# Performance work log

Measured on AMD Instinct MI355X. Metric: run time of the kernel, lower is better.

## Reference

```python
import jax, jax.numpy as jnp
import numpy as np

B, H, S, D = 4, 16, 2048, 64
SCALE = 8.0  # sqrt(D)
NEG = -1000000000.0


def setup_inputs() -> dict:
    key = jax.random.key(0)
    kq, kk, kv = jax.random.split(key, 3)
    q = jax.random.normal(kq, (B, H, S, D), dtype=jnp.float32)
    k = jax.random.normal(kk, (B, H, S, D), dtype=jnp.float32)
    v = jax.random.normal(kv, (B, H, S, D), dtype=jnp.float32)
    # causal mask: True means masked out (matches torch masked_fill)
    mask = jnp.triu(jnp.ones((S, S), dtype=bool), k=1)[None, None, :, :]
    mask = jnp.broadcast_to(mask, (B, 1, S, S))
    return {"q": q, "k": k, "v": v, "mask": mask}


def reference(q, k, v, mask):
    # score = q @ k^T / scale  -> [B,H,S,S]
    score = jnp.einsum("bhqd,bhkd->bhqk", q, k) / SCALE
    score = jnp.where(mask, NEG, score)
    probs = jax.nn.softmax(score, axis=-1)
    context = jnp.einsum("bhqk,bhkd->bhqd", probs, v)
    return context
```

## Files before the change

kernel.cpp:

```cpp
#include <hip/hip_runtime.h>

#define SQ 2048
#define DH 64
#define BK 64
#define NQT 32
#define NBH 64
#define M0 8.0f

#define WS_BYTES ((size_t)2 * NBH * SQ * DH * 2)

typedef float f32x4 __attribute__((ext_vector_type(4)));
typedef __bf16 bf16x8 __attribute__((ext_vector_type(8)));
typedef _Float16 f16x4 __attribute__((ext_vector_type(4)));
typedef __fp16 fp16x2 __attribute__((ext_vector_type(2)));
typedef unsigned short u16x8 __attribute__((ext_vector_type(8)));
typedef unsigned int u32x4 __attribute__((ext_vector_type(4)));

static __device__ __forceinline__ unsigned int pkbf(float a, float b) {
#if __has_builtin(__builtin_amdgcn_cvt_pk_bf16_f32)
  typedef __bf16 bf16x2 __attribute__((ext_vector_type(2)));
  bf16x2 r = __builtin_amdgcn_cvt_pk_bf16_f32(a, b);
  return __builtin_bit_cast(unsigned int, r);
#else
  unsigned int ua = __builtin_bit_cast(unsigned int, a);
  unsigned int ub = __builtin_bit_cast(unsigned int, b);
  ua += 0x7fffu + ((ua >> 16) & 1u);
  ub += 0x7fffu + ((ub >> 16) & 1u);
  return (ua >> 16) | (ub & 0xffff0000u);
#endif
}

static __device__ __forceinline__ unsigned int pkf16(float a, float b) {
  fp16x2 r = __builtin_amdgcn_cvt_pkrtz(a, b);
  return __builtin_bit_cast(unsigned int, r);
}

static __device__ __forceinline__ f32x4 mfma_qk(u16x8 a, u16x8 b, f32x4 c) {
  return __builtin_amdgcn_mfma_f32_16x16x32_bf16(
      __builtin_bit_cast(bf16x8, a), __builtin_bit_cast(bf16x8, b), c, 0, 0, 0);
}

static __device__ __forceinline__ f32x4 mfma_pv(f16x4 a, f16x4 b, f32x4 c) {
  return __builtin_amdgcn_mfma_f32_16x16x16f16(a, b, c, 0, 0, 0);
}

static __device__ __forceinline__ void ld16(unsigned short* l, const unsigned short* g) {
  __builtin_amdgcn_global_load_lds(
      (const __attribute__((address_space(1))) unsigned int*)(const void*)g,
      (__attribute__((address_space(3))) unsigned int*)(void*)l, 16, 0, 0);
}

static __device__ __forceinline__ void store_tile(float* wb, float* dst,
                                                  const f32x4* o, int lane,
                                                  int l15, int quad) {
#pragma unroll
  for (int dt = 0; dt < 4; ++dt) {
    const int colw = dt * 16 + quad * 4;
    *(f32x4*)&wb[l15 * 64 + (colw ^ ((l15 & 3) * 16))] = o[dt];
  }
  __builtin_amdgcn_wave_barrier();
#pragma unroll
  for (int j = 0; j < 4; ++j) {
    const int row = j * 4 + (lane >> 4);
    const int colw = (lane & 15) * 4;
    f32x4 v = *(const f32x4*)&wb[row * 64 + (colw ^ ((row & 3) * 16))];
    *(f32x4*)&dst[row * 64 + colw] = v;
  }
}

__global__ __launch_bounds__(256) void prep(const float* __restrict__ K,
                                            const float* __restrict__ V,
                                            unsigned short* __restrict__ Kb,
                                            unsigned short* __restrict__ Vt) {
  const int bh = (int)blockIdx.x >> 5;
  const int st = (int)blockIdx.x & 31;
  const int tid = threadIdx.x;
  __shared__ __align__(16) unsigned short T[DH * 64];
  {
    const int r = tid >> 2, c0 = (tid & 3) * 16;
    const float* kp = K + ((size_t)bh * SQ + st * 64 + r) * DH + c0;
    f32x4 x0 = *(const f32x4*)kp, x1 = *(const f32x4*)(kp + 4),
          x2 = *(const f32x4*)(kp + 8), x3 = *(const f32x4*)(kp + 12);
    u32x4 w0 = {pkbf(x0[0], x0[1]), pkbf(x0[2], x0[3]), pkbf(x1[0], x1[1]), pkbf(x1[2], x1[3])};
    u32x4 w1 = {pkbf(x2[0], x2[1]), pkbf(x2[2], x2[3]), pkbf(x3[0], x3[1]), pkbf(x3[2], x3[3])};
    unsigned short* kb = Kb + ((size_t)bh * SQ + st * 64 + r) * DH + c0;
    *(u32x4*)kb = w0;
    *(u32x4*)(kb + 8) = w1;
  }
  {
    const int kvb = (tid >> 4) * 4, vdb = (tid & 15) * 4;
    const float* vp = V + ((size_t)bh * SQ + st * 64 + kvb) * DH + vdb;
    f32x4 r0 = *(const f32x4*)vp, r1 = *(const f32x4*)(vp + DH),
          r2 = *(const f32x4*)(vp + 2 * DH), r3 = *(const f32x4*)(vp + 3 * DH);
    const int uu = kvb >> 3, h = (kvb >> 2) & 1;
#pragma unroll
    for (int i = 0; i < 4; ++i) {
      const int d = vdb + i;
      uint2 w = {pkf16(r0[i], r1[i]), pkf16(r2[i], r3[i])};
      *(uint2*)&T[d * 64 + ((uu ^ (d & 7)) * 8) + h * 4] = w;
    }
  }
  __syncthreads();
  {
    const int d2 = tid >> 2, cp = (tid & 3) * 2;
#pragma unroll
    for (int e = 0; e < 2; ++e) {
      const int uu = cp + e;
      u16x8 val = *(const u16x8*)&T[d2 * 64 + ((uu ^ (d2 & 7)) * 8)];
      *(u16x8*)&Vt[(size_t)bh * DH * SQ + (size_t)d2 * SQ + st * 64 + uu * 8] = val;
    }
  }
}

__global__ __launch_bounds__(256, 4) void fa_main(
    const float* __restrict__ Q, const unsigned short* __restrict__ Kb,
    const unsigned short* __restrict__ Vt, float* __restrict__ O) {
  const int lin = (int)blockIdx.x;
  const int xcd = lin & 7, u = lin >> 3;
  const int hh = u & 7;
  const int pi = (int)((0x32104567BA98CDEFull >> ((u >> 3) * 4)) & 15u);
  const int bh = hh * 8 + xcd;
  const int tend = 2 * pi + 1;

  const int tid = threadIdx.x;
  const int wv = tid >> 6;
  const int lane = tid & 63;
  const int l15 = lane & 15;
  const int quad = lane >> 4;

  __shared__ __align__(16) unsigned short S0[2 * BK * DH];
  __shared__ __align__(16) unsigned short S1[2 * BK * DH];

  const size_t hq = (size_t)bh * (SQ * DH);
  const unsigned short* KbH = Kb + (size_t)bh * SQ * DH;
  const unsigned short* VtH = Vt + (size_t)bh * DH * SQ;

  const int srow = wv * 16 + (lane >> 3);
  const int sc = lane & 7;

  const int qbase = pi * 128 + wv * 32;
  const int dtw = 2 * pi + (wv >> 1);
  const int qo = (wv & 1) * 32;

  u16x8 qf[2][2];
  {
    const float scq = 0.125f * 1.4426950408889634f;
#pragma unroll
    for (int f = 0; f < 2; ++f) {
      const float* qp = Q + hq + (size_t)(qbase + 16 * f + l15) * DH + quad * 8;
#pragma unroll
      for (int c = 0; c < 2; ++c) {
        f32x4 x = *(const f32x4*)(qp + c * 32);
        f32x4 y = *(const f32x4*)(qp + c * 32 + 4);
        u32x4 w = {pkbf(x[0] * scq, x[1] * scq), pkbf(x[2] * scq, x[3] * scq),
                   pkbf(y[0] * scq, y[1] * scq), pkbf(y[2] * scq, y[3] * scq)};
        qf[f][c] = __builtin_bit_cast(u16x8, w);
      }
    }
  }

  f32x4 o0[4], o1[4], la0, la1;
#pragma unroll
  for (int dt = 0; dt < 4; ++dt) {
    o0[dt] = (f32x4){0.f, 0.f, 0.f, 0.f};
    o1[dt] = (f32x4){0.f, 0.f, 0.f, 0.f};
  }
  la0 = (f32x4){0.f, 0.f, 0.f, 0.f};
  la1 = (f32x4){0.f, 0.f, 0.f, 0.f};
  const f16x4 ones = {(_Float16)1.f, (_Float16)1.f, (_Float16)1.f, (_Float16)1.f};

  auto stage = [&](unsigned short* W, int t) {
    const int kb = t * BK;
    unsigned short* Kd = W;
    unsigned short* Vd = W + BK * DH;
#pragma unroll
    for (int j = 0; j < 2; ++j) {
      const int row = srow + j * 8;
      ld16(&Kd[row * 64 + sc * 8], &KbH[(size_t)(kb + row) * 64 + ((sc ^ (row & 7)) * 8)]);
      ld16(&Vd[row * 64 + sc * 8], &VtH[(size_t)row * SQ + kb + ((sc ^ (row & 7)) * 8)]);
    }
  };

  auto attend = [&](const unsigned short* R, bool diag) {
    const unsigned short* Ks = R;
    const unsigned short* Vs = R + BK * DH;
    f32x4 s0[4], s1[4];
#pragma unroll
    for (int nt = 0; nt < 4; ++nt) {
      f32x4 a0 = {-M0, -M0, -M0, -M0}, a1 = {-M0, -M0, -M0, -M0};
#pragma unroll
      for (int c = 0; c < 2; ++c) {
        const int row = nt * 16 + l15;
        const int un = c * 4 + quad;
        u16x8 kf = *(const u16x8*)&Ks[row * 64 + ((un ^ (row & 7)) * 8)];
        a0 = mfma_qk(kf, qf[0][c], a0);
        a1 = mfma_qk(kf, qf[1][c], a1);
      }
      s0[nt] = a0;
      s1[nt] = a1;
    }
    if (diag) {
#pragma unroll
      for (int nt = 0; nt < 4; ++nt)
#pragma unroll
        for (int r = 0; r < 4; ++r) {
          const int kvl = nt * 16 + quad * 4 + r;
          if (kvl > qo + l15) s0[nt][r] = -1e30f;
          if (kvl > qo + 16 + l15) s1[nt][r] = -1e30f;
        }
    }
    f16x4 pf0[4], pf1[4];
#pragma unroll
    for (int nt = 0; nt < 4; ++nt) {
      f32x4 p0, p1;
#pragma unroll
      for (int r = 0; r < 4; ++r) {
        p0[r] = __builtin_amdgcn_exp2f(s0[nt][r]);
        p1[r] = __builtin_amdgcn_exp2f(s1[nt][r]);
      }
      uint2 w0 = {pkf16(p0[0], p0[1]), pkf16(p0[2], p0[3])};
      uint2 w1 = {pkf16(p1[0], p1[1]), pkf16(p1[2], p1[3])};
      pf0[nt] = __builtin_bit_cast(f16x4, w0);
      pf1[nt] = __builtin_bit_cast(f16x4, w1);
    }
#pragma unroll
    for (int nt = 0; nt < 4; ++nt) {
      la0 = mfma_pv(ones, pf0[nt], la0);
      la1 = mfma_pv(ones, pf1[nt], la1);
    }
#pragma unroll
    for (int dt = 0; dt < 4; ++dt) {
      const int d = dt * 16 + l15;
#pragma unroll
      for (int nt = 0; nt < 4; ++nt) {
        const int uv = nt * 2 + (quad >> 1);
        f16x4 vf = *(const f16x4*)&Vs[d * 64 + ((uv ^ (d & 7)) * 8) + (quad & 1) * 4];
        o0[dt] = mfma_pv(vf, pf0[nt], o0[dt]);
        o1[dt] = mfma_pv(vf, pf1[nt], o1[dt]);
      }
    }
  };

  auto step = [&](int t, const unsigned short* R, unsigned short* W) {
    if (t <= dtw) attend(R, t == dtw);
    __syncthreads();
    if (t + 2 <= tend) stage(W, t + 2);
  };

  stage(S0, 0);
  __syncthreads();
  stage(S1, 1);
  for (int t = 0; t <= tend; t += 2) {
    step(t, S0, S0);
    if (t + 1 <= tend) step(t + 1, S1, S1);
  }

  float* wb = (float*)S0 + wv * 1024;
  {
    const float inv = 1.0f / la0[0];
    f32x4 on[4];
#pragma unroll
    for (int dt = 0; dt < 4; ++dt) on[dt] = o0[dt] * inv;
    store_tile(wb, O + hq + (size_t)(qbase)*DH, on, lane, l15, quad);
  }
  {
    const float inv = 1.0f / la1[0];
    f32x4 on[4];
#pragma unroll
    for (int dt = 0; dt < 4; ++dt) on[dt] = o1[dt] * inv;
    store_tile(wb, O + hq + (size_t)(qbase + 16) * DH, on, lane, l15, quad);
  }
}

__global__ __launch_bounds__(256, 4) void fa_full(
    const float* __restrict__ Q, const float* __restrict__ K,
    const float* __restrict__ V, float* __restrict__ O) {
  const int lin = (int)blockIdx.x;
  const int xcd = lin & 7;
  const int u = lin >> 3;
  const int hh = u & 7;
  const int p = u >> 3;
  const int bh = hh * 8 + xcd;
  const int tid = threadIdx.x;
  const int wv = tid >> 6;
  const int lane = tid & 63;
  const int l15 = lane & 15;
  const int quad = lane >> 4;
  __shared__ __align__(16) unsigned short SMEM[2][2 * BK * DH];
  const size_t hbase = (size_t)bh * (SQ * DH);
  const int krr = tid >> 3, kcc = (tid & 7) * 8;
  const int kvb = (tid >> 4) * 4, vdb = (tid & 15) * 4;
#pragma unroll
  for (int ph = 0; ph < 2; ++ph) {
    const int qt = ph ? (NQT - 1 - p) : p;
    const int wq0 = qt * 64 + wv * 16;
    u16x8 qf[2];
    {
      const float scq = 0.125f * 1.4426950408889634f;
      const float* qp = Q + hbase + (size_t)(wq0 + l15) * DH + quad * 8;
#pragma unroll
      for (int c = 0; c < 2; ++c) {
        f32x4 x = *(const f32x4*)(qp + c * 32);
        f32x4 y = *(const f32x4*)(qp + c * 32 + 4);
        u32x4 w = {pkbf(x[0] * scq, x[1] * scq), pkbf(x[2] * scq, x[3] * scq),
                   pkbf(y[0] * scq, y[1] * scq), pkbf(y[2] * scq, y[3] * scq)};
        qf[c] = __builtin_bit_cast(u16x8, w);
      }
    }
    f32x4 o[4];
#pragma unroll
    for (int dt = 0; dt < 4; ++dt) o[dt] = (f32x4){0.f, 0.f, 0.f, 0.f};
    float l = 0.f;
    f32x4 ka[2][2], va[4];
    {
      const float* kp = K + hbase + (size_t)krr * DH + kcc;
      ka[0][0] = *(const f32x4*)kp;             ka[0][1] = *(const f32x4*)(kp + 4);
      ka[1][0] = *(const f32x4*)(kp + 32 * DH); ka[1][1] = *(const f32x4*)(kp + 32 * DH + 4);
      const float* vp = V + hbase + (size_t)kvb * DH + vdb;
      va[0] = *(const f32x4*)vp;            va[1] = *(const f32x4*)(vp + DH);
      va[2] = *(const f32x4*)(vp + 2 * DH); va[3] = *(const f32x4*)(vp + 3 * DH);
    }
    __syncthreads();
    {
      unsigned short* Ksn = SMEM[0];
      unsigned short* Vsn = SMEM[0] + BK * DH;
#pragma unroll
      for (int h = 0; h < 2; ++h) {
        const int rr = h * 32 + krr;
        u32x4 w = {pkbf(ka[h][0][0], ka[h][0][1]), pkbf(ka[h][0][2], ka[h][0][3]),
                   pkbf(ka[h][1][0], ka[h][1][1]), pkbf(ka[h][1][2], ka[h][1][3])};
        *(u32x4*)&Ksn[rr * DH + (kcc ^ ((rr & 7) * 8))] = w;
      }
#pragma unroll
      for (int i = 0; i < 4; ++i) {
        const int d = vdb + i;
        uint2 w = {pkf16(va[0][i], va[1][i]), pkf16(va[2][i], va[3][i])};
        *(uint2*)&Vsn[d * BK + (kvb ^ ((d & 15) * 4))] = w;
      }
    }
    __syncthreads();
    for (int t = 0; t <= qt; ++t) {
      const unsigned short* Ks = SMEM[t & 1];
      const unsigned short* Vs = SMEM[t & 1] + BK * DH;
      if (t < qt) {
        const int kb2 = (t + 1) * BK;
        const float* kp = K + hbase + (size_t)(kb2 + krr) * DH + kcc;
        ka[0][0] = *(const f32x4*)kp;             ka[0][1] = *(const f32x4*)(kp + 4);
        ka[1][0] = *(const f32x4*)(kp + 32 * DH); ka[1][1] = *(const f32x4*)(kp + 32 * DH + 4);
        const float* vp = V + hbase + (size_t)(kb2 + kvb) * DH + vdb;
        va[0] = *(const f32x4*)vp;            va[1] = *(const f32x4*)(vp + DH);
        va[2] = *(const f32x4*)(vp + 2 * DH); va[3] = *(const f32x4*)(vp + 3 * DH);
      }
      f32x4 s[4];
#pragma unroll
      for (int nt = 0; nt < 4; ++nt) {
        f32x4 acc = {-M0, -M0, -M0, -M0};
#pragma unroll
        for (int c = 0; c < 2; ++c) {
          const int row = nt * 16 + l15;
          u16x8 kf = *(const u16x8*)&Ks[row * DH + ((c * 32 + quad * 8) ^ ((l15 & 7) * 8))];
          acc = mfma_qk(kf, qf[c], acc);
        }
        s[nt] = acc;
      }
      if (t == qt) {
#pragma unroll
        for (int nt = 0; nt < 4; ++nt)
#pragma unroll
          for (int r = 0; r < 4; ++r)
            if (nt * 16 + quad * 4 + r > wv * 16 + l15) s[nt][r] = -1e30f;
      }
      f16x4 pf[4];
#pragma unroll
      for (int nt = 0; nt < 4; ++nt) {
        f32x4 pr;
#pragma unroll
        for (int r = 0; r < 4; ++r) { pr[r] = __builtin_amdgcn_exp2f(s[nt][r]); l += pr[r]; }
        uint2 w2 = {pkf16(pr[0], pr[1]), pkf16(pr[2], pr[3])};
        pf[nt] = __builtin_bit_cast(f16x4, w2);
      }
#pragma unroll
      for (int dt = 0; dt < 4; ++dt) {
        const int d = dt * 16 + l15;
#pragma unroll
        for (int nt = 0; nt < 4; ++nt) {
          f16x4 vf = *(const f16x4*)&Vs[d * BK + ((nt * 16 + quad * 4) ^ (l15 * 4))];
          o[dt] = mfma_pv(vf, pf[nt], o[dt]);
        }
      }
      if (t < qt) {
        unsigned short* Ksn = SMEM[(t + 1) & 1];
        unsigned short* Vsn = SMEM[(t + 1) & 1] + BK * DH;
#pragma unroll
        for (int h = 0; h < 2; ++h) {
          const int rr = h * 32 + krr;
          u32x4 w = {pkbf(ka[h][0][0], ka[h][0][1]), pkbf(ka[h][0][2], ka[h][0][3]),
                     pkbf(ka[h][1][0], ka[h][1][1]), pkbf(ka[h][1][2], ka[h][1][3])};
          *(u32x4*)&Ksn[rr * DH + (kcc ^ ((rr & 7) * 8))] = w;
        }
#pragma unroll
        for (int i = 0; i < 4; ++i) {
          const int d = vdb + i;
          uint2 w = {pkf16(va[0][i], va[1][i]), pkf16(va[2][i], va[3][i])};
          *(uint2*)&Vsn[d * BK + (kvb ^ ((d & 15) * 4))] = w;
        }
        __syncthreads();
      }
    }
    l += __shfl_xor(l, 16, 64);
    l += __shfl_xor(l, 32, 64);
    const float inv = 1.0f / l;
    f32x4 on[4];
#pragma unroll
    for (int dt = 0; dt < 4; ++dt) on[dt] = o[dt] * inv;
    float* wb = (float*)SMEM[(qt + 1) & 1] + wv * 1024;
    store_tile(wb, O + hbase + (size_t)wq0 * DH, on, lane, l15, quad);
  }
}

extern "C" void kernel_launch(void* const* d_in, const int* in_sizes, int n_in,
                              void* d_out, int out_size, void* d_ws, size_t ws_size,
                              hipStream_t stream) {
  const float* q = (const float*)d_in[0];
  const float* k = (const float*)d_in[1];
  const float* v = (const float*)d_in[2];
  float* o = (float*)d_out;
  if (ws_size >= WS_BYTES) {
    unsigned short* Kb = (unsigned short*)d_ws;
    unsigned short* Vt = Kb + (size_t)NBH * SQ * DH;
    prep<<<dim3(NBH * 32), 256, 0, stream>>>(k, v, Kb, Vt);
    fa_main<<<dim3(1024), 256, 0, stream>>>(q, Kb, Vt, o);
  } else {
    fa_full<<<dim3(1024), 256, 0, stream>>>(q, k, v, o);
  }
}
```

Measured before the change: 210.2 us.

## Use 16x16x32 f16 MFMA for PV with permuted K row staging

Switches the P·V and row-sum matrix ops from 16x16x16 f16 MFMA to the 16x16x32 f16 variant, halving the number of MFMA issues per tile. To make the QK output layout match the 8-wide k operand, K rows are permuted when staged into shared memory. The causal-mask index is remapped to match. V fragments are now read as 8-wide vectors. It relies on the permutation being consistent across the mask, the probability packing and the V reads.

```diff
diff --git a/kernel.cpp b/kernel.cpp
--- a/kernel.cpp
+++ b/kernel.cpp
@@ -12,6 +12,7 @@
 typedef float f32x4 __attribute__((ext_vector_type(4)));
 typedef __bf16 bf16x8 __attribute__((ext_vector_type(8)));
 typedef _Float16 f16x4 __attribute__((ext_vector_type(4)));
+typedef _Float16 f16x8 __attribute__((ext_vector_type(8)));
 typedef __fp16 fp16x2 __attribute__((ext_vector_type(2)));
 typedef unsigned short u16x8 __attribute__((ext_vector_type(8)));
 typedef unsigned int u32x4 __attribute__((ext_vector_type(4)));
@@ -44,6 +45,10 @@
   return __builtin_amdgcn_mfma_f32_16x16x16f16(a, b, c, 0, 0, 0);
 }
 
+static __device__ __forceinline__ f32x4 mfma_pv32(f16x8 a, f16x8 b, f32x4 c) {
+  return __builtin_amdgcn_mfma_f32_16x16x32_f16(a, b, c, 0, 0, 0);
+}
+
 static __device__ __forceinline__ void ld16(unsigned short* l, const unsigned short* g) {
   __builtin_amdgcn_global_load_lds(
       (const __attribute__((address_space(1))) unsigned int*)(const void*)g,
@@ -167,7 +172,8 @@
   }
   la0 = (f32x4){0.f, 0.f, 0.f, 0.f};
   la1 = (f32x4){0.f, 0.f, 0.f, 0.f};
-  const f16x4 ones = {(_Float16)1.f, (_Float16)1.f, (_Float16)1.f, (_Float16)1.f};
+  const f16x8 ones8 = {(_Float16)1.f, (_Float16)1.f, (_Float16)1.f, (_Float16)1.f,
+                       (_Float16)1.f, (_Float16)1.f, (_Float16)1.f, (_Float16)1.f};
 
   auto stage = [&](unsigned short* W, int t) {
     const int kb = t * BK;
@@ -175,9 +181,10 @@
     unsigned short* Vd = W + BK * DH;
 #pragma unroll
     for (int j = 0; j < 2; ++j) {
-      const int row = srow + j * 8;
-      ld16(&Kd[row * 64 + sc * 8], &KbH[(size_t)(kb + row) * 64 + ((sc ^ (row & 7)) * 8)]);
-      ld16(&Vd[row * 64 + sc * 8], &VtH[(size_t)row * SQ + kb + ((sc ^ (row & 7)) * 8)]);
+      const int p = srow + j * 8;
+      const int kp = (p & ~31) | (((p >> 2) & 3) << 3) | (((p >> 4) & 1) << 2) | (p & 3);
+      ld16(&Kd[p * 64 + sc * 8], &KbH[(size_t)(kb + kp) * 64 + ((sc ^ (p & 7)) * 8)]);
+      ld16(&Vd[p * 64 + sc * 8], &VtH[(size_t)p * SQ + kb + ((sc ^ (p & 7)) * 8)]);
     }
   };
 
@@ -204,39 +211,43 @@
       for (int nt = 0; nt < 4; ++nt)
 #pragma unroll
         for (int r = 0; r < 4; ++r) {
-          const int kvl = nt * 16 + quad * 4 + r;
+          const int kvl = (nt >> 1) * 32 + quad * 8 + (nt & 1) * 4 + r;
           if (kvl > qo + l15) s0[nt][r] = -1e30f;
           if (kvl > qo + 16 + l15) s1[nt][r] = -1e30f;
         }
     }
-    f16x4 pf0[4], pf1[4];
-#pragma unroll
-    for (int nt = 0; nt < 4; ++nt) {
-      f32x4 p0, p1;
+    f16x8 pf0[2], pf1[2];
+#pragma unroll
+    for (int n2 = 0; n2 < 2; ++n2) {
+      f32x4 pe0, po0, pe1, po1;
 #pragma unroll
       for (int r = 0; r < 4; ++r) {
-        p0[r] = __builtin_amdgcn_exp2f(s0[nt][r]);
-        p1[r] = __builtin_amdgcn_exp2f(s1[nt][r]);
-      }
-      uint2 w0 = {pkf16(p0[0], p0[1]), pkf16(p0[2], p0[3])};
-      uint2 w1 = {pkf16(p1[0], p1[1]), pkf16(p1[2], p1[3])};
-      pf0[nt] = __builtin_bit_cast(f16x4, w0);
-      pf1[nt] = __builtin_bit_cast(f16x4, w1);
-    }
-#pragma unroll
-    for (int nt = 0; nt < 4; ++nt) {
-      la0 = mfma_pv(ones, pf0[nt], la0);
-      la1 = mfma_pv(ones, pf1[nt], la1);
+        pe0[r] = __builtin_amdgcn_exp2f(s0[2 * n2][r]);
+        po0[r] = __builtin_amdgcn_exp2f(s0[2 * n2 + 1][r]);
+        pe1[r] = __builtin_amdgcn_exp2f(s1[2 * n2][r]);
+        po1[r] = __builtin_amdgcn_exp2f(s1[2 * n2 + 1][r]);
+      }
+      u32x4 w0 = {pkf16(pe0[0], pe0[1]), pkf16(pe0[2], pe0[3]),
+                  pkf16(po0[0], po0[1]), pkf16(po0[2], po0[3])};
+      u32x4 w1 = {pkf16(pe1[0], pe1[1]), pkf16(pe1[2], pe1[3]),
+                  pkf16(po1[0], po1[1]), pkf16(po1[2], po1[3])};
+      pf0[n2] = __builtin_bit_cast(f16x8, w0);
+      pf1[n2] = __builtin_bit_cast(f16x8, w1);
+    }
+#pragma unroll
+    for (int n2 = 0; n2 < 2; ++n2) {
+      la0 = mfma_pv32(ones8, pf0[n2], la0);
+      la1 = mfma_pv32(ones8, pf1[n2], la1);
     }
 #pragma unroll
     for (int dt = 0; dt < 4; ++dt) {
       const int d = dt * 16 + l15;
 #pragma unroll
-      for (int nt = 0; nt < 4; ++nt) {
-        const int uv = nt * 2 + (quad >> 1);
-        f16x4 vf = *(const f16x4*)&Vs[d * 64 + ((uv ^ (d & 7)) * 8) + (quad & 1) * 4];
-        o0[dt] = mfma_pv(vf, pf0[nt], o0[dt]);
-        o1[dt] = mfma_pv(vf, pf1[nt], o1[dt]);
+      for (int n2 = 0; n2 < 2; ++n2) {
+        const int uv = n2 * 4 + quad;
+        f16x8 vf = *(const f16x8*)&Vs[d * 64 + ((uv ^ (d & 7)) * 8)];
+        o0[dt] = mfma_pv32(vf, pf0[n2], o0[dt]);
+        o1[dt] = mfma_pv32(vf, pf1[n2], o1[dt]);
       }
     }
   };
```

Result: faster. 202.6 us (-3.6%).
